# Performance work log

Measured on AMD Instinct MI355X. Metric: run time of the kernel, lower is better.

Reference implementation:

```python
import jax, jax.numpy as jnp
import numpy as np

DEPTH, D, HEADS, PS, C_IN = 12, 1024, 8, 16, 1
B, H, W = 8, 512, 512


def setup_inputs() -> dict:
    key = jax.random.key(0)
    ks = jax.random.split(key, 8)
    s = 0.02
    rn = lambda k, shp: jax.random.normal(k, shp, jnp.float32) * s
    return dict(
        x=jax.random.normal(ks[0], (B, C_IN, H, W), jnp.float32),
        conv_w=rn(ks[1], (D, C_IN, PS, PS)),
        conv_b=jnp.zeros((D,), jnp.float32),
        ln1_g=jnp.ones((DEPTH, D), jnp.float32),
        ln1_b=jnp.zeros((DEPTH, D), jnp.float32),
        qkv_w=rn(ks[2], (DEPTH, 3 * D, D)),
        qkv_b=jnp.zeros((DEPTH, 3 * D), jnp.float32),
        proj_w=rn(ks[3], (DEPTH, D, D)),
        proj_b=jnp.zeros((DEPTH, D), jnp.float32),
        ln2_g=jnp.ones((DEPTH, D), jnp.float32),
        ln2_b=jnp.zeros((DEPTH, D), jnp.float32),
        fc1_w=rn(ks[4], (DEPTH, 2 * D, D)),
        fc1_b=jnp.zeros((DEPTH, 2 * D), jnp.float32),
        fc2_w=rn(ks[5], (DEPTH, D, 2 * D)),
        fc2_b=jnp.zeros((DEPTH, D), jnp.float32),
    )


def _layernorm(x, g, b, eps=1e-5):
    m = x.mean(-1, keepdims=True)
    v = ((x - m) ** 2).mean(-1, keepdims=True)
    return (x - m) * jax.lax.rsqrt(v + eps) * g + b


def _pos_encoding(n, d):
    # faithful to the source: angle = pos / 10000 ** (2*i/d) with i the EVEN index
    pos = jnp.arange(n, dtype=jnp.float32)[:, None]
    i_even = jnp.arange(0, d, 2, dtype=jnp.float32)
    ang = pos / (10000.0 ** (2.0 * i_even / d))
    return jnp.stack([jnp.sin(ang), jnp.cos(ang)], axis=-1).reshape(n, d)


def reference(x, conv_w, conv_b, ln1_g, ln1_b, qkv_w, qkv_b, proj_w, proj_b,
              ln2_g, ln2_b, fc1_w, fc1_b, fc2_w, fc2_b):
    b = x.shape[0]
    Hp, Wp = H // PS, W // PS
    n = Hp * Wp  # 1024 tokens
    hd = D // HEADS
    scale = float(hd) ** -0.5

    # patch embed: conv with stride == kernel  ==  per-patch matmul
    patches = x.reshape(b, C_IN, Hp, PS, Wp, PS).transpose(0, 2, 4, 1, 3, 5)
    patches = patches.reshape(b, n, C_IN * PS * PS)
    tok = patches @ conv_w.reshape(D, -1).T + conv_b
    tok = tok + _pos_encoding(n, D)

    def step(t, p):
        g1, b1, qw, qb, pw, pb, g2, b2, f1w, f1b, f2w, f2b = p
        h = _layernorm(t, g1, b1)
        qkv = (h @ qw.T + qb).reshape(b, n, 3, HEADS, hd).transpose(2, 0, 3, 1, 4)
        q, k, v = qkv[0], qkv[1], qkv[2]  # [b, heads, n, hd]
        att = jax.nn.softmax(jnp.einsum('bhqd,bhkd->bhqk', q, k) * scale, axis=-1)
        o = jnp.einsum('bhqk,bhkd->bhqd', att, v).transpose(0, 2, 1, 3).reshape(b, n, D)
        t = t + o @ pw.T + pb
        h = _layernorm(t, g2, b2)
        h = jax.nn.gelu(h @ f1w.T + f1b, approximate=False)
        t = t + h @ f2w.T + f2b
        return t, None

    tok, _ = jax.lax.scan(step, tok, (ln1_g, ln1_b, qkv_w, qkv_b, proj_w, proj_b,
                                      ln2_g, ln2_b, fc1_w, fc1_b, fc2_w, fc2_b))

    # reconstruction: tok -> (b, 4, ps*ps, Hp, Wp); scatter fina[:,:,i::ps,j::ps] = x[:,:,k]
    x4 = tok.reshape(b, n, D // 4, 4).transpose(0, 3, 2, 1).reshape(b, 4, PS, PS, Hp, Wp)
    fina = x4.transpose(0, 1, 4, 2, 5, 3).reshape(b, 4, H, W)  # fina[b,c,a*ps+i,bb*ps+j]
    # rearrange 'b (h w) p1 p2 -> b 1 (p1 h) (p2 w)' with h=w=2
    out = fina.reshape(b, 2, 2, H, W).transpose(0, 3, 1, 4, 2).reshape(b, 1, 2 * H, 2 * W)
    return out
```

## Files before the change

kernel.cpp:

```cpp
#include <hip/hip_runtime.h>
#include <hip/hip_bf16.h>
#include <stdint.h>

typedef unsigned short u16;
typedef __attribute__((ext_vector_type(8))) __bf16 bf16x8;
typedef __attribute__((ext_vector_type(4))) float  f32x4;

__device__ __forceinline__ float bf2f(u16 v) {
    union { unsigned int u; float f; } x; x.u = ((unsigned int)v) << 16; return x.f;
}
__device__ __forceinline__ u16 f2bf(float f) {
    union { float f; unsigned int u; } x; x.f = f;
    unsigned int u = x.u;
    unsigned int lsb = (u >> 16) & 1u;
    u += 0x7fffu + lsb;
    return (u16)(u >> 16);
}

#define GLDS16(gp, lp)                                                         \
    __builtin_amdgcn_global_load_lds(                                          \
        (const __attribute__((address_space(1))) void*)(gp),                   \
        (__attribute__((address_space(3))) void*)(lp), 16, 0, 0)

__global__ __launch_bounds__(256) void cvt_kernel(const float* __restrict__ src,
                                                  u16* __restrict__ dst, int n4)
{
    int gid = blockIdx.x * 256 + threadIdx.x;
    if (gid < n4) {
        float4 v = ((const float4*)src)[gid];
        ushort4 o;
        o.x = f2bf(v.x); o.y = f2bf(v.y); o.z = f2bf(v.z); o.w = f2bf(v.w);
        ((ushort4*)dst)[gid] = o;
    }
}

__global__ __launch_bounds__(256) void cvt4_kernel(
    const float* __restrict__ s0, const float* __restrict__ s1,
    const float* __restrict__ s2, const float* __restrict__ s3,
    u16* __restrict__ d0, u16* __restrict__ d1,
    u16* __restrict__ d2, u16* __restrict__ d3)
{
    int gid = blockIdx.x * 256 + threadIdx.x;
    const float* s; u16* d; int idx;
    if (gid < 786432)                { s = s0; d = d0; idx = gid; }
    else if (gid < 1048576)          { s = s1; d = d1; idx = gid - 786432; }
    else if (gid < 1572864)          { s = s2; d = d2; idx = gid - 1048576; }
    else                             { s = s3; d = d3; idx = gid - 1572864; }
    float4 v = ((const float4*)s)[idx];
    ushort4 o;
    o.x = f2bf(v.x); o.y = f2bf(v.y); o.z = f2bf(v.z); o.w = f2bf(v.w);
    ((ushort4*)d)[idx] = o;
}

__global__ __launch_bounds__(256) void gemm_bt(
    const u16* __restrict__ A, const u16* __restrict__ B,
    const float* __restrict__ bias, const float* __restrict__ res,
    void* __restrict__ Cout, int c_fp32,
    int K, int lda, int ldb, int ldc, int ldres,
    long long sA1, long long sA2, long long sB1, long long sB2,
    long long sC1, long long sC2, int zinner, float scale, int act)
{
    __shared__ u16 As[128 * 32];
    __shared__ u16 Bs[128 * 32];

    int z  = blockIdx.z;
    int z1 = z / zinner;
    int z2 = z - z1 * zinner;
    A += z1 * sA1 + z2 * sA2;
    B += z1 * sB1 + z2 * sB2;
    long long coff = z1 * sC1 + z2 * sC2;

    int n0 = blockIdx.x << 7;
    int m0 = blockIdx.y << 7;

    int t = threadIdx.x;
    int w = t >> 6, l = t & 63;
    int wm = w >> 1, wn = w & 1;

    const u16* Ab = A + (long long)(m0 + w * 16 + (l >> 2)) * lda + ((l & 3) << 3);
    const u16* Bb = B + (long long)(n0 + w * 16 + (l >> 2)) * ldb + ((l & 3) << 3);
    long long a64 = (long long)64 * lda;
    long long b64 = (long long)64 * ldb;
    u16* AsW = &As[w << 9];
    u16* BsW = &Bs[w << 9];

    f32x4 acc[4][4];
#pragma unroll
    for (int i = 0; i < 4; i++)
#pragma unroll
        for (int j = 0; j < 4; j++)
            acc[i][j] = (f32x4){0.f, 0.f, 0.f, 0.f};

    int lk = (l >> 4) << 3;
    int lr = l & 15;

    for (int k0 = 0; k0 < K; k0 += 32) {
        GLDS16(Ab + k0,        AsW);
        GLDS16(Ab + k0 + a64,  AsW + 2048);
        GLDS16(Bb + k0,        BsW);
        GLDS16(Bb + k0 + b64,  BsW + 2048);
        __syncthreads();

        bf16x8 av[4], bv[4];
#pragma unroll
        for (int i = 0; i < 4; i++)
            av[i] = *(const bf16x8*)&As[((wm << 6) + (i << 4) + lr) * 32 + lk];
#pragma unroll
        for (int j = 0; j < 4; j++)
            bv[j] = *(const bf16x8*)&Bs[((wn << 6) + (j << 4) + lr) * 32 + lk];
#pragma unroll
        for (int i = 0; i < 4; i++)
#pragma unroll
            for (int j = 0; j < 4; j++)
                acc[i][j] = __builtin_amdgcn_mfma_f32_16x16x32_bf16(av[i], bv[j], acc[i][j], 0, 0, 0);
        __syncthreads();
    }

    int rq = (l >> 4) << 2;
#pragma unroll
    for (int j = 0; j < 4; j++) {
        int col = n0 + (wn << 6) + (j << 4) + lr;
        float bvv = bias ? bias[col] : 0.f;
#pragma unroll
        for (int i = 0; i < 4; i++) {
#pragma unroll
            for (int r = 0; r < 4; r++) {
                int row = m0 + (wm << 6) + (i << 4) + rq + r;
                float v = acc[i][j][r] * scale + bvv;
                if (act) v = 0.5f * v * (1.f + erff(v * 0.70710678118654752f));
                if (res) v += res[(long long)row * ldres + col];
                long long idx = coff + (long long)row * ldc + col;
                if (c_fp32) ((float*)Cout)[idx] = v;
                else        ((u16*)Cout)[idx]  = f2bf(v);
            }
        }
    }
}

#define ASCALE 0.08838834764831845f

__global__ __launch_bounds__(256) void attn_kernel(
    const u16* __restrict__ qkv, const u16* __restrict__ vt,
    u16* __restrict__ out)
{
    __shared__ __align__(16) u16 Ks[64 * 128];
    __shared__ __align__(16) u16 Vs[128 * 64];
    __shared__ __align__(16) u16 Ps[4][32 * 72];

    int bh = blockIdx.y; int b = bh >> 3, hd = bh & 7;
    int q0 = blockIdx.x << 7;
    int t = threadIdx.x, w = t >> 6, l = t & 63;
    int lg = l >> 4, lr = l & 15;

    const u16* qp = qkv + ((long long)(b * 1024 + q0 + (w << 5) + lr)) * 3072
                        + hd * 128 + (lg << 3);
    bf16x8 qf[2][4];
#pragma unroll
    for (int rb = 0; rb < 2; rb++)
#pragma unroll
        for (int kf = 0; kf < 4; kf++)
            qf[rb][kf] = *(const bf16x8*)(qp + rb * 16 * 3072 + (kf << 5));

    const u16* kg = qkv + ((long long)(b * 1024)) * 3072 + 1024 + hd * 128;
    const u16* vg = vt + (long long)bh * 131072;
    u16* Pw = &Ps[w][0];

    f32x4 oa[2][8];
#pragma unroll
    for (int rb = 0; rb < 2; rb++)
#pragma unroll
        for (int db = 0; db < 8; db++)
            oa[rb][db] = (f32x4){0.f, 0.f, 0.f, 0.f};
    float m_run[2][4], l_run[2][4];
#pragma unroll
    for (int rb = 0; rb < 2; rb++)
#pragma unroll
        for (int r = 0; r < 4; r++) { m_run[rb][r] = -1e30f; l_run[rb][r] = 0.f; }

    for (int kv0 = 0; kv0 < 1024; kv0 += 64) {
#pragma unroll
        for (int i = 0; i < 4; i++) {
            int ck   = (((w << 2) + i) << 6) + l;
            int krow = ck >> 4;
            int kslot = (ck & 15) ^ (krow & 7);
            GLDS16(kg + (long long)(kv0 + krow) * 3072 + (kslot << 3),
                   Ks + (((w << 2) + i) << 9));
            int vd   = ck >> 3;
            int vslot = (ck & 7) ^ (vd & 7);
            GLDS16(vg + (long long)vd * 1024 + kv0 + (vslot << 3),
                   Vs + (((w << 2) + i) << 9));
        }
        __syncthreads();

        f32x4 s[2][4];
#pragma unroll
        for (int kb = 0; kb < 4; kb++) {
            s[0][kb] = (f32x4){0.f, 0.f, 0.f, 0.f};
            s[1][kb] = (f32x4){0.f, 0.f, 0.f, 0.f};
        }
#pragma unroll
        for (int kf = 0; kf < 4; kf++)
#pragma unroll
            for (int kb = 0; kb < 4; kb++) {
                bf16x8 bk = *(const bf16x8*)
                    &Ks[(((kb << 4) + lr) << 7) + (((((kf << 2) + lg)) ^ (lr & 7)) << 3)];
                s[0][kb] = __builtin_amdgcn_mfma_f32_16x16x32_bf16(qf[0][kf], bk, s[0][kb], 0, 0, 0);
                s[1][kb] = __builtin_amdgcn_mfma_f32_16x16x32_bf16(qf[1][kf], bk, s[1][kb], 0, 0, 0);
            }

#pragma unroll
        for (int rb = 0; rb < 2; rb++) {
            float mx[4], al[4], rs[4];
#pragma unroll
            for (int r = 0; r < 4; r++)
                mx[r] = fmaxf(fmaxf(s[rb][0][r], s[rb][1][r]),
                              fmaxf(s[rb][2][r], s[rb][3][r]));
#pragma unroll
            for (int mask = 1; mask < 16; mask <<= 1)
#pragma unroll
                for (int r = 0; r < 4; r++)
                    mx[r] = fmaxf(mx[r], __shfl_xor(mx[r], mask));
#pragma unroll
            for (int r = 0; r < 4; r++) {
                float mn = fmaxf(m_run[rb][r], mx[r] * ASCALE);
                al[r] = __expf(m_run[rb][r] - mn);
                m_run[rb][r] = mn;
                rs[r] = 0.f;
            }
#pragma unroll
            for (int kb = 0; kb < 4; kb++)
#pragma unroll
                for (int r = 0; r < 4; r++) {
                    float p = __expf(s[rb][kb][r] * ASCALE - m_run[rb][r]);
                    rs[r] += p;
                    Pw[((rb << 4) + (lg << 2) + r) * 72 + (kb << 4) + lr] = f2bf(p);
                }
#pragma unroll
            for (int mask = 1; mask < 16; mask <<= 1)
#pragma unroll
                for (int r = 0; r < 4; r++)
                    rs[r] += __shfl_xor(rs[r], mask);
#pragma unroll
            for (int r = 0; r < 4; r++)
                l_run[rb][r] = l_run[rb][r] * al[r] + rs[r];
#pragma unroll
            for (int db = 0; db < 8; db++)
#pragma unroll
                for (int r = 0; r < 4; r++)
                    oa[rb][db][r] *= al[r];
        }

#pragma unroll
        for (int ks = 0; ks < 2; ks++) {
            bf16x8 pa0 = *(const bf16x8*)&Pw[lr * 72 + (ks << 5) + (lg << 3)];
            bf16x8 pa1 = *(const bf16x8*)&Pw[(16 + lr) * 72 + (ks << 5) + (lg << 3)];
#pragma unroll
            for (int db = 0; db < 8; db++) {
                bf16x8 vf = *(const bf16x8*)
                    &Vs[(((db << 4) + lr) << 6) + ((((ks << 2) + lg) ^ (lr & 7)) << 3)];
                oa[0][db] = __builtin_amdgcn_mfma_f32_16x16x32_bf16(pa0, vf, oa[0][db], 0, 0, 0);
                oa[1][db] = __builtin_amdgcn_mfma_f32_16x16x32_bf16(pa1, vf, oa[1][db], 0, 0, 0);
            }
        }
        __syncthreads();
    }

    long long obase = ((long long)(b * 1024 + q0 + (w << 5)) << 10) + hd * 128;
#pragma unroll
    for (int rb = 0; rb < 2; rb++) {
        float il[4];
#pragma unroll
        for (int r = 0; r < 4; r++) il[r] = 1.f / l_run[rb][r];
#pragma unroll
        for (int db = 0; db < 8; db++)
#pragma unroll
            for (int r = 0; r < 4; r++)
                out[obase + (long long)((rb << 4) + (lg << 2) + r) * 1024
                          + (db << 4) + lr] = f2bf(oa[rb][db][r] * il[r]);
    }
}

__global__ __launch_bounds__(256) void patches_kernel(const float* __restrict__ x,
                                                      u16* __restrict__ p)
{
    int gid = blockIdx.x * 256 + threadIdx.x;
    int c = gid & 255, tk = gid >> 8;
    int b = tk >> 10, n = tk & 1023;
    int ph = n >> 5, pw = n & 31;
    int i = c >> 4, j = c & 15;
    p[gid] = f2bf(x[((long long)b << 18) + (long long)(ph * 16 + i) * 512 + pw * 16 + j]);
}

__global__ __launch_bounds__(256) void posenc_kernel(float* __restrict__ tok)
{
    int gid = blockIdx.x * 256 + threadIdx.x;
    int d = gid & 1023;
    int n = (gid >> 10) & 1023;
    int j = d >> 1;
    float ang = (float)n * exp2f(-13.287712379549449f * (float)j * (1.0f / 256.0f));
    float pe = (d & 1) ? cosf(ang) : sinf(ang);
    tok[gid] += pe;
}

__global__ __launch_bounds__(256) void ln_kernel(const float* __restrict__ x,
                                                 const float* __restrict__ g,
                                                 const float* __restrict__ b,
                                                 u16* __restrict__ y)
{
    int row = blockIdx.x, t = threadIdx.x;
    const float* xr = x + (long long)row * 1024;
    float v[4]; float s = 0.f, ss = 0.f;
#pragma unroll
    for (int i = 0; i < 4; i++) { v[i] = xr[i * 256 + t]; s += v[i]; ss += v[i] * v[i]; }
    __shared__ float rs[256], rss[256];
    rs[t] = s; rss[t] = ss; __syncthreads();
    for (int o = 128; o > 0; o >>= 1) {
        if (t < o) { rs[t] += rs[t + o]; rss[t] += rss[t + o]; }
        __syncthreads();
    }
    float mean = rs[0] * (1.f / 1024.f);
    float var  = rss[0] * (1.f / 1024.f) - mean * mean;
    float rstd = rsqrtf(var + 1e-5f);
    u16* yr = y + (long long)row * 1024;
#pragma unroll
    for (int i = 0; i < 4; i++) {
        int d = i * 256 + t;
        yr[d] = f2bf((v[i] - mean) * rstd * g[d] + b[d]);
    }
}

__global__ __launch_bounds__(256) void vt_kernel(const u16* __restrict__ qkv,
                                                 u16* __restrict__ vt)
{
    int bh   = blockIdx.x >> 4;
    int tile = blockIdx.x & 15;
    int b = bh >> 3, hd = bh & 7;
    int t = threadIdx.x;
    __shared__ u16 tl[64][130];
    int nk0 = tile * 64;
    int dcol = t & 127, r0 = t >> 7;
    const u16* src = qkv + ((long long)(b * 1024 + nk0)) * 3072 + 2048 + hd * 128 + dcol;
#pragma unroll
    for (int r = 0; r < 32; r++) {
        int nk = r0 + r * 2;
        tl[nk][dcol] = src[(long long)nk * 3072];
    }
    __syncthreads();
    u16* dst = vt + ((long long)bh * 128) * 1024 + nk0;
#pragma unroll
    for (int r = 0; r < 32; r++) {
        int flat = r * 256 + t;
        int d = flat >> 6, nk = flat & 63;
        dst[(long long)d * 1024 + nk] = tl[nk][d];
    }
}

__global__ __launch_bounds__(256) void recon_kernel(const float* __restrict__ tok,
                                                    float* __restrict__ out)
{
    int gid = blockIdx.x * 256 + threadIdx.x;
    int b  = gid >> 20;
    int y  = (gid >> 10) & 1023;
    int xx = gid & 1023;
    int p1 = y & 1,  hh = y >> 1,  a  = hh >> 4, i = hh & 15;
    int p2 = xx & 1, wv = xx >> 1, bb = wv >> 4, j = wv & 15;
    int n = a * 32 + bb;
    int d = ((i * 16 + j) << 2) + (p1 << 1) + p2;
    out[gid] = tok[((long long)(b * 1024 + n) << 10) + d];
}

extern "C" void kernel_launch(void* const* d_in, const int* in_sizes, int n_in,
                              void* d_out, int out_size, void* d_ws, size_t ws_size,
                              hipStream_t stream)
{
    (void)in_sizes; (void)n_in; (void)out_size; (void)ws_size;
    const float* x      = (const float*)d_in[0];
    const float* conv_w = (const float*)d_in[1];
    const float* conv_b = (const float*)d_in[2];
    const float* ln1_g  = (const float*)d_in[3];
    const float* ln1_b  = (const float*)d_in[4];
    const float* qkv_w  = (const float*)d_in[5];
    const float* qkv_b  = (const float*)d_in[6];
    const float* proj_w = (const float*)d_in[7];
    const float* proj_b = (const float*)d_in[8];
    const float* ln2_g  = (const float*)d_in[9];
    const float* ln2_b  = (const float*)d_in[10];
    const float* fc1_w  = (const float*)d_in[11];
    const float* fc1_b  = (const float*)d_in[12];
    const float* fc2_w  = (const float*)d_in[13];
    const float* fc2_b  = (const float*)d_in[14];

    char* ws = (char*)d_ws;
    float* tokf  = (float*)ws;
    u16* h       = (u16*)(ws + 33554432);
    u16* qkvb    = (u16*)(ws + 50331648);
    u16* vt      = (u16*)(ws + 100663296);
    u16* attnout = (u16*)(ws + 117440512);
    u16* mid     = (u16*)(ws + 134217728);
    u16* patches = (u16*)(ws + 167772160);
    u16* convw   = (u16*)(ws + 171966464);
    u16* wqkv    = (u16*)(ws + 172490752);
    u16* wproj   = (u16*)(ws + 178782208);
    u16* wfc1    = (u16*)(ws + 180879360);
    u16* wfc2    = (u16*)(ws + 185073664);

    dim3 blk(256);

    patches_kernel<<<dim3(8192), blk, 0, stream>>>(x, patches);
    cvt_kernel<<<dim3(256), blk, 0, stream>>>(conv_w, convw, 65536);
    gemm_bt<<<dim3(8, 64, 1), blk, 0, stream>>>(
        patches, convw, conv_b, (const float*)nullptr, (void*)tokf, 1,
        256, 256, 256, 1024, 0, 0LL, 0LL, 0LL, 0LL, 0LL, 0LL, 1, 1.0f, 0);
    posenc_kernel<<<dim3(32768), blk, 0, stream>>>(tokf);

    for (int L = 0; L < 12; L++) {
        cvt4_kernel<<<dim3(8192), blk, 0, stream>>>(
            qkv_w + (long long)L * 3145728, proj_w + (long long)L * 1048576,
            fc1_w + (long long)L * 2097152, fc2_w + (long long)L * 2097152,
            wqkv, wproj, wfc1, wfc2);

        ln_kernel<<<dim3(8192), blk, 0, stream>>>(
            tokf, ln1_g + L * 1024, ln1_b + L * 1024, h);

        gemm_bt<<<dim3(24, 64, 1), blk, 0, stream>>>(
            h, wqkv, qkv_b + L * 3072,
            (const float*)nullptr, (void*)qkvb, 0,
            1024, 1024, 1024, 3072, 0, 0LL, 0LL, 0LL, 0LL, 0LL, 0LL, 1, 1.0f, 0);

        vt_kernel<<<dim3(1024), blk, 0, stream>>>(qkvb, vt);

        attn_kernel<<<dim3(8, 64, 1), blk, 0, stream>>>(qkvb, vt, attnout);

        gemm_bt<<<dim3(8, 64, 1), blk, 0, stream>>>(
            attnout, wproj, proj_b + L * 1024,
            tokf, (void*)tokf, 1,
            1024, 1024, 1024, 1024, 1024, 0LL, 0LL, 0LL, 0LL, 0LL, 0LL, 1, 1.0f, 0);

        ln_kernel<<<dim3(8192), blk, 0, stream>>>(
            tokf, ln2_g + L * 1024, ln2_b + L * 1024, h);

        gemm_bt<<<dim3(16, 64, 1), blk, 0, stream>>>(
            h, wfc1, fc1_b + L * 2048,
            (const float*)nullptr, (void*)mid, 0,
            1024, 1024, 1024, 2048, 0, 0LL, 0LL, 0LL, 0LL, 0LL, 0LL, 1, 1.0f, 1);

        gemm_bt<<<dim3(8, 64, 1), blk, 0, stream>>>(
            mid, wfc2, fc2_b + L * 1024,
            tokf, (void*)tokf, 1,
            2048, 2048, 2048, 1024, 1024, 0LL, 0LL, 0LL, 0LL, 0LL, 0LL, 1, 1.0f, 0);
    }

    recon_kernel<<<dim3(32768), blk, 0, stream>>>(tokf, (float*)d_out);
}
```

Baseline: 5.350 ms.

## Replace GEMM with 8-wave 128x256 tile, 4-stage LDS pipeline and swizzle

Replaces the single-buffered 128x128 GEMM with a 512-thread kernel using 128x256 output tiles. A 4-deep LDS ring is fed by async global-to-LDS loads, with explicit vmcnt waits and barriers so loads overlap MFMA work. It also XOR-swizzles LDS rows to avoid bank conflicts, remaps workgroup IDs for L2 locality, and raises MFMA priority with setprio. The batched-z stride support is dropped. This adds LDS use (96KB) and hand-tuned wait counts that only hold for K being a multiple of 32 and at least 96.

```diff
diff --git a/kernel.cpp b/kernel.cpp
--- a/kernel.cpp
+++ b/kernel.cpp
@@ -52,37 +52,42 @@
     ((ushort4*)d)[idx] = o;
 }
 
-__global__ __launch_bounds__(256) void gemm_bt(
+__global__ __launch_bounds__(512, 2) void gemm8p(
     const u16* __restrict__ A, const u16* __restrict__ B,
     const float* __restrict__ bias, const float* __restrict__ res,
     void* __restrict__ Cout, int c_fp32,
-    int K, int lda, int ldb, int ldc, int ldres,
-    long long sA1, long long sA2, long long sB1, long long sB2,
-    long long sC1, long long sC2, int zinner, float scale, int act)
-{
-    __shared__ u16 As[128 * 32];
-    __shared__ u16 Bs[128 * 32];
-
-    int z  = blockIdx.z;
-    int z1 = z / zinner;
-    int z2 = z - z1 * zinner;
-    A += z1 * sA1 + z2 * sA2;
-    B += z1 * sB1 + z2 * sB2;
-    long long coff = z1 * sC1 + z2 * sC2;
-
-    int n0 = blockIdx.x << 7;
-    int m0 = blockIdx.y << 7;
+    int K, int lda, int ldb, int ldc, int ldres, float scale, int act)
+{
+    __shared__ __align__(16) u16 As[4][128 * 32];
+    __shared__ __align__(16) u16 Bs[4][256 * 32];
+
+    int nt = K >> 5;
+
+    int gx  = gridDim.x;
+    int nwg = gx * gridDim.y;
+    int bid = blockIdx.y * gx + blockIdx.x;
+    int cpx = nwg >> 3;
+    int swz = (bid & 7) * cpx + (bid >> 3);
+    int m0 = (swz / gx) << 7;
+    int n0 = (swz % gx) << 8;
 
     int t = threadIdx.x;
     int w = t >> 6, l = t & 63;
-    int wm = w >> 1, wn = w & 1;
-
-    const u16* Ab = A + (long long)(m0 + w * 16 + (l >> 2)) * lda + ((l & 3) << 3);
-    const u16* Bb = B + (long long)(n0 + w * 16 + (l >> 2)) * ldb + ((l & 3) << 3);
-    long long a64 = (long long)64 * lda;
-    long long b64 = (long long)64 * ldb;
-    u16* AsW = &As[w << 9];
-    u16* BsW = &Bs[w << 9];
+    int wm = w >> 2, wn = w & 3;
+    int lg = l >> 4, lr = l & 15;
+
+    int arow = t >> 2, aslot = t & 3;
+    const u16* Ag  = A + (long long)(m0 + arow) * lda + ((aslot ^ ((arow >> 1) & 3)) << 3);
+    const u16* Bg0 = B + (long long)(n0 + arow) * ldb + ((aslot ^ ((arow >> 1) & 3)) << 3);
+    const u16* Bg1 = Bg0 + (long long)128 * ldb;
+
+#define STAGE_A(tt)  GLDS16(Ag  + ((long long)(tt) << 5), &As[(tt) & 3][w << 9])
+#define STAGE_B0(tt) GLDS16(Bg0 + ((long long)(tt) << 5), &Bs[(tt) & 3][w << 9])
+#define STAGE_B1(tt) GLDS16(Bg1 + ((long long)(tt) << 5), &Bs[(tt) & 3][4096 + (w << 9)])
+
+    int sx = lg ^ ((lr >> 1) & 3);
+    const u16* Asr = &As[0][0] + (wm << 11) + (lr << 5) + (sx << 3);
+    const u16* Bsr = &Bs[0][0] + (wn << 11) + (lr << 5) + (sx << 3);
 
     f32x4 acc[4][4];
 #pragma unroll
@@ -91,32 +96,60 @@
         for (int j = 0; j < 4; j++)
             acc[i][j] = (f32x4){0.f, 0.f, 0.f, 0.f};
 
-    int lk = (l >> 4) << 3;
-    int lr = l & 15;
-
-    for (int k0 = 0; k0 < K; k0 += 32) {
-        GLDS16(Ab + k0,        AsW);
-        GLDS16(Ab + k0 + a64,  AsW + 2048);
-        GLDS16(Bb + k0,        BsW);
-        GLDS16(Bb + k0 + b64,  BsW + 2048);
-        __syncthreads();
-
-        bf16x8 av[4], bv[4];
-#pragma unroll
-        for (int i = 0; i < 4; i++)
-            av[i] = *(const bf16x8*)&As[((wm << 6) + (i << 4) + lr) * 32 + lk];
-#pragma unroll
-        for (int j = 0; j < 4; j++)
-            bv[j] = *(const bf16x8*)&Bs[((wn << 6) + (j << 4) + lr) * 32 + lk];
-#pragma unroll
-        for (int i = 0; i < 4; i++)
-#pragma unroll
-            for (int j = 0; j < 4; j++)
-                acc[i][j] = __builtin_amdgcn_mfma_f32_16x16x32_bf16(av[i], bv[j], acc[i][j], 0, 0, 0);
-        __syncthreads();
-    }
-
-    int rq = (l >> 4) << 2;
+    STAGE_A(0); STAGE_B0(0); STAGE_B1(0);
+    if (nt > 1) { STAGE_A(1); STAGE_B0(1); STAGE_B1(1); }
+    if (nt > 2) { STAGE_A(2); STAGE_B0(2); STAGE_B1(2); }
+    asm volatile("s_waitcnt vmcnt(6)" ::: "memory");
+    __builtin_amdgcn_s_barrier();
+    __builtin_amdgcn_sched_barrier(0);
+
+    for (int tt = 0; tt < nt; ++tt) {
+        int buf = tt & 3;
+        const u16* Ab = Asr + (buf << 12);
+        const u16* Bb = Bsr + (buf << 13);
+
+        bf16x8 av[4], bv0[2];
+#pragma unroll
+        for (int i = 0; i < 4; i++) av[i]  = *(const bf16x8*)(Ab + i * 512);
+#pragma unroll
+        for (int j = 0; j < 2; j++) bv0[j] = *(const bf16x8*)(Bb + j * 512);
+        if (tt + 3 < nt) { STAGE_A(tt + 3); STAGE_B0(tt + 3); }
+        __builtin_amdgcn_s_barrier();
+        __builtin_amdgcn_sched_barrier(0);
+        __builtin_amdgcn_s_setprio(1);
+#pragma unroll
+        for (int j = 0; j < 2; j++)
+#pragma unroll
+            for (int i = 0; i < 4; i++)
+                acc[i][j] = __builtin_amdgcn_mfma_f32_16x16x32_bf16(av[i], bv0[j], acc[i][j], 0, 0, 0);
+        __builtin_amdgcn_s_setprio(0);
+        __builtin_amdgcn_s_barrier();
+        __builtin_amdgcn_sched_barrier(0);
+
+        bf16x8 bv1[2];
+#pragma unroll
+        for (int j = 0; j < 2; j++) bv1[j] = *(const bf16x8*)(Bb + (2 + j) * 512);
+        if (tt + 3 < nt) STAGE_B1(tt + 3);
+        __builtin_amdgcn_s_barrier();
+        __builtin_amdgcn_sched_barrier(0);
+        __builtin_amdgcn_s_setprio(1);
+#pragma unroll
+        for (int j = 0; j < 2; j++)
+#pragma unroll
+            for (int i = 0; i < 4; i++)
+                acc[i][2 + j] = __builtin_amdgcn_mfma_f32_16x16x32_bf16(av[i], bv1[j], acc[i][2 + j], 0, 0, 0);
+        __builtin_amdgcn_s_setprio(0);
+        if (tt < nt - 3)       asm volatile("s_waitcnt vmcnt(6)" ::: "memory");
+        else if (tt == nt - 3) asm volatile("s_waitcnt vmcnt(3)" ::: "memory");
+        else if (tt == nt - 2) asm volatile("s_waitcnt vmcnt(0)" ::: "memory");
+        __builtin_amdgcn_s_barrier();
+        __builtin_amdgcn_sched_barrier(0);
+    }
+#undef STAGE_A
+#undef STAGE_B0
+#undef STAGE_B1
+
+    int rq = lg << 2;
 #pragma unroll
     for (int j = 0; j < 4; j++) {
         int col = n0 + (wn << 6) + (j << 4) + lr;
@@ -129,7 +162,7 @@
                 float v = acc[i][j][r] * scale + bvv;
                 if (act) v = 0.5f * v * (1.f + erff(v * 0.70710678118654752f));
                 if (res) v += res[(long long)row * ldres + col];
-                long long idx = coff + (long long)row * ldc + col;
+                long long idx = (long long)row * ldc + col;
                 if (c_fp32) ((float*)Cout)[idx] = v;
                 else        ((u16*)Cout)[idx]  = f2bf(v);
             }
@@ -405,12 +438,13 @@
     u16* wfc2    = (u16*)(ws + 185073664);
 
     dim3 blk(256);
+    dim3 blk512(512);
 
     patches_kernel<<<dim3(8192), blk, 0, stream>>>(x, patches);
     cvt_kernel<<<dim3(256), blk, 0, stream>>>(conv_w, convw, 65536);
-    gemm_bt<<<dim3(8, 64, 1), blk, 0, stream>>>(
+    gemm8p<<<dim3(4, 64), blk512, 0, stream>>>(
         patches, convw, conv_b, (const float*)nullptr, (void*)tokf, 1,
-        256, 256, 256, 1024, 0, 0LL, 0LL, 0LL, 0LL, 0LL, 0LL, 1, 1.0f, 0);
+        256, 256, 256, 1024, 0, 1.0f, 0);
     posenc_kernel<<<dim3(32768), blk, 0, stream>>>(tokf);
 
     for (int L = 0; L < 12; L++) {
@@ -422,32 +456,28 @@
         ln_kernel<<<dim3(8192), blk, 0, stream>>>(
             tokf, ln1_g + L * 1024, ln1_b + L * 1024, h);
 
-        gemm_bt<<<dim3(24, 64, 1), blk, 0, stream>>>(
-            h, wqkv, qkv_b + L * 3072,
-            (const float*)nullptr, (void*)qkvb, 0,
-            1024, 1024, 1024, 3072, 0, 0LL, 0LL, 0LL, 0LL, 0LL, 0LL, 1, 1.0f, 0);
+        gemm8p<<<dim3(12, 64), blk512, 0, stream>>>(
+            h, wqkv, qkv_b + L * 3072, (const float*)nullptr, (void*)qkvb, 0,
+            1024, 1024, 1024, 3072, 0, 1.0f, 0);
 
         vt_kernel<<<dim3(1024), blk, 0, stream>>>(qkvb, vt);
 
         attn_kernel<<<dim3(8, 64, 1), blk, 0, stream>>>(qkvb, vt, attnout);
 
-        gemm_bt<<<dim3(8, 64, 1), blk, 0, stream>>>(
-            attnout, wproj, proj_b + L * 1024,
-            tokf, (void*)tokf, 1,
-            1024, 1024, 1024, 1024, 1024, 0LL, 0LL, 0LL, 0LL, 0LL, 0LL, 1, 1.0f, 0);
+        gemm8p<<<dim3(4, 64), blk512, 0, stream>>>(
+            attnout, wproj, proj_b + L * 1024, tokf, (void*)tokf, 1,
+            1024, 1024, 1024, 1024, 1024, 1.0f, 0);
 
         ln_kernel<<<dim3(8192), blk, 0, stream>>>(
             tokf, ln2_g + L * 1024, ln2_b + L * 1024, h);
 
-        gemm_bt<<<dim3(16, 64, 1), blk, 0, stream>>>(
-            h, wfc1, fc1_b + L * 2048,
-            (const float*)nullptr, (void*)mid, 0,
-            1024, 1024, 1024, 2048, 0, 0LL, 0LL, 0LL, 0LL, 0LL, 0LL, 1, 1.0f, 1);
-
-        gemm_bt<<<dim3(8, 64, 1), blk, 0, stream>>>(
-            mid, wfc2, fc2_b + L * 1024,
-            tokf, (void*)tokf, 1,
-            2048, 2048, 2048, 1024, 1024, 0LL, 0LL, 0LL, 0LL, 0LL, 0LL, 1, 1.0f, 0);
+        gemm8p<<<dim3(8, 64), blk512, 0, stream>>>(
+            h, wfc1, fc1_b + L * 2048, (const float*)nullptr, (void*)mid, 0,
+            1024, 1024, 1024, 2048, 0, 1.0f, 1);
+
+        gemm8p<<<dim3(4, 64), blk512, 0, stream>>>(
+            mid, wfc2, fc2_b + L * 1024, tokf, (void*)tokf, 1,
+            2048, 2048, 2048, 1024, 1024, 1.0f, 0);
     }
 
     recon_kernel<<<dim3(32768), blk, 0, stream>>>(tokf, (float*)d_out);
```

New measurement: 4.915 ms. 8.1% less time.
